# Optimization experiments

Measured on AMD Instinct MI355X. Metric: run time of the kernel, lower is better.

## Reference

```python
import jax, jax.numpy as jnp
import numpy as np

B, SQ, SKV, D, DC, R, H = 4, 2048, 2048, 1024, 1024, 4, 16


def setup_inputs() -> dict:
    key = jax.random.key(0)
    ks = jax.random.split(key, 15)
    s = 0.02
    return {
        "hidden_states": jax.random.normal(ks[0], (B, SQ, D), jnp.float32),
        "encoder_hidden_states": jax.random.normal(ks[1], (B, SKV, DC), jnp.float32),
        "Wq": jax.random.normal(ks[2], (D, D), jnp.float32) * s,
        "Wk": jax.random.normal(ks[3], (DC, D), jnp.float32) * s,
        "Wv": jax.random.normal(ks[4], (DC, D), jnp.float32) * s,
        "Wo": jax.random.normal(ks[5], (D, D), jnp.float32) * s,
        "bo": jax.random.normal(ks[6], (D,), jnp.float32) * s,
        "q_lora_down": jax.random.normal(ks[7], (D, R), jnp.float32) * s,
        "q_lora_up": jax.random.normal(ks[8], (R, D), jnp.float32) * s,
        "k_lora_down": jax.random.normal(ks[9], (DC, R), jnp.float32) * s,
        "k_lora_up": jax.random.normal(ks[10], (R, D), jnp.float32) * s,
        "v_lora_down": jax.random.normal(ks[11], (DC, R), jnp.float32) * s,
        "v_lora_up": jax.random.normal(ks[12], (R, D), jnp.float32) * s,
        "out_lora_down": jax.random.normal(ks[13], (D, R), jnp.float32) * s,
        "out_lora_up": jax.random.normal(ks[14], (R, D), jnp.float32) * s,
        "n_heads": H,
    }


def reference(hidden_states, encoder_hidden_states, Wq, Wk, Wv, Wo, bo,
              q_lora_down, q_lora_up, k_lora_down, k_lora_up,
              v_lora_down, v_lora_up, out_lora_down, out_lora_up, n_heads):
    b, sq, d = hidden_states.shape
    skv = encoder_hidden_states.shape[1]
    hd = d // n_heads
    scale = 1.0 / jnp.sqrt(jnp.asarray(hd, hidden_states.dtype))

    # Q/K/V projections with LoRA adapters (bias-free, diffusers style)
    q = hidden_states @ Wq + (hidden_states @ q_lora_down) @ q_lora_up
    k = encoder_hidden_states @ Wk + (encoder_hidden_states @ k_lora_down) @ k_lora_up
    v = encoder_hidden_states @ Wv + (encoder_hidden_states @ v_lora_down) @ v_lora_up

    q = q.reshape(b, sq, n_heads, hd)
    k = k.reshape(b, skv, n_heads, hd)
    v = v.reshape(b, skv, n_heads, hd)

    # get_attention_scores: scaled QK^T + softmax (no mask)
    scores = jnp.einsum("bqhd,bkhd->bhqk", q, k) * scale
    probs = jax.nn.softmax(scores, axis=-1)

    out = jnp.einsum("bhqk,bkhd->bqhd", probs, v).reshape(b, sq, d)

    # to_out[0] linear + LoRA on the pre-projection residual; to_out[1] dropout is identity
    residual = out
    out = out @ Wo + bo + (residual @ out_lora_down) @ out_lora_up
    return out
```

## Files before the change

### kernel.cpp

```cpp
#include <hip/hip_runtime.h>
#include <hip/hip_bf16.h>

typedef __attribute__((ext_vector_type(8))) short bf16x8;
typedef __attribute__((ext_vector_type(4))) float f32x4;

#define DEVFN static __device__ __forceinline__

constexpr int kSQ = 2048, kSKV = 2048, kD = 1024, kH = 16;
constexpr int kM = 4 * kSQ;

DEVFN unsigned short f2bf(float f) {
  union { float f; unsigned u; } v; v.f = f;
  unsigned r = v.u + 0x7FFFu + ((v.u >> 16) & 1u);
  return (unsigned short)(r >> 16);
}
DEVFN float bf2f(unsigned short h) {
  union { unsigned u; float f; } v; v.u = ((unsigned)h) << 16; return v.f;
}
DEVFN unsigned cvtpk(float lo, float hi) {
  unsigned r;
  asm("v_cvt_pk_bf16_f32 %0, %1, %2" : "=v"(r) : "v"(lo), "v"(hi));
  return r;
}
DEVFN float vexp2(float x) {
  float r;
  asm("v_exp_f32 %0, %1" : "=v"(r) : "v"(x));
  return r;
}

DEVFN void gload16(const void* g, void* l) {
  __builtin_amdgcn_global_load_lds(
      (const __attribute__((address_space(1))) unsigned int*)g,
      (__attribute__((address_space(3))) unsigned int*)l, 16, 0, 0);
}

#define WT12 asm volatile("s_waitcnt vmcnt(12)" ::: "memory")
#define WT6  asm volatile("s_waitcnt vmcnt(6)" ::: "memory")
#define WT0  asm volatile("s_waitcnt vmcnt(0)" ::: "memory")

__global__ __launch_bounds__(256) void k_prep_wt(
    const float* __restrict__ hs, const float* __restrict__ enc,
    const float* __restrict__ Wq, const float* __restrict__ Wk,
    const float* __restrict__ Wv, const float* __restrict__ Wo,
    unsigned short* __restrict__ hsb, unsigned short* __restrict__ encb,
    unsigned short* __restrict__ Wqt, unsigned short* __restrict__ Wkvt,
    unsigned short* __restrict__ Wot) {
  __shared__ unsigned short tile[64][65];
  const int bid = blockIdx.x;
  const int tid = threadIdx.x;

  if (bid < 2 * kM) {
    const bool isH = bid < kM;
    const int rr = isH ? bid : bid - kM;
    const float* srcRow = (isH ? hs : enc) + (size_t)rr * kD;
    unsigned short* dstRow = (isH ? hsb : encb) + (size_t)rr * kD;
    float4 x = reinterpret_cast<const float4*>(srcRow)[tid];
    short4 o;
    o.x = (short)f2bf(x.x); o.y = (short)f2bf(x.y);
    o.z = (short)f2bf(x.z); o.w = (short)f2bf(x.w);
    *reinterpret_cast<short4*>(dstRow + tid * 4) = o;
  } else {
    const int t = bid - 2 * kM;
    const int wid = t >> 8, tt = t & 255;
    const float* W = (wid == 0) ? Wq : (wid == 1) ? Wk : (wid == 2) ? Wv : Wo;
    unsigned short* Wt = (wid == 0) ? Wqt : (wid == 1) ? Wkvt
                        : (wid == 2) ? (Wkvt + (size_t)1024 * 1024) : Wot;
    const int tk0 = (tt & 15) * 64;
    const int tn0 = (tt >> 4) * 64;
    for (int i = tid; i < 4096; i += 256) {
      int r = i >> 6, c = i & 63;
      tile[r][c] = f2bf(W[(size_t)(tk0 + r) * 1024 + tn0 + c]);
    }
    __syncthreads();
    for (int i = tid; i < 4096; i += 256) {
      int r = i >> 6, c = i & 63;
      Wt[(size_t)(tn0 + r) * 1024 + tk0 + c] = tile[c][r];
    }
  }
}

__global__ __launch_bounds__(256) void k_lora(
    const unsigned short* __restrict__ X,
    const float* __restrict__ dn0, const float* __restrict__ dn1,
    float* __restrict__ tout, int tstr) {
  __shared__ unsigned short DNT[16][1032];
  const int tid = threadIdx.x;
  const int rbase = (int)blockIdx.x * 64;
  for (int i = tid; i < 16 * 1032; i += 256) DNT[i / 1032][i % 1032] = 0;
  __syncthreads();
  for (int i = tid; i < 4096; i += 256) {
    const int k = i >> 2, c = i & 3;
    DNT[c][k] = f2bf(dn0[i]);
  }
  if (dn1 != nullptr) {
    for (int i = tid; i < 4096; i += 256) {
      const int k = i >> 2, c = i & 3;
      DNT[4 + c][k] = f2bf(dn1[i]);
    }
  }
  __syncthreads();
  const int l = tid & 63, w = tid >> 6;
  const int lr = l & 15, lk = l >> 4;
  const unsigned short* Xr = X + (size_t)(rbase + w * 16 + lr) * 1024 + lk * 8;
  const f32x4 zero = {0.f, 0.f, 0.f, 0.f};
  f32x4 acc0 = zero, acc1 = zero;
#pragma unroll 4
  for (int k0 = 0; k0 < 1024; k0 += 64) {
    bf16x8 a0 = *(const bf16x8*)(Xr + k0);
    bf16x8 b0 = *(const bf16x8*)&DNT[lr][k0 + lk * 8];
    bf16x8 a1 = *(const bf16x8*)(Xr + k0 + 32);
    bf16x8 b1 = *(const bf16x8*)&DNT[lr][k0 + 32 + lk * 8];
    acc0 = __builtin_amdgcn_mfma_f32_16x16x32_bf16(a0, b0, acc0, 0, 0, 0);
    acc1 = __builtin_amdgcn_mfma_f32_16x16x32_bf16(a1, b1, acc1, 0, 0, 0);
  }
  if (lr < tstr) {
#pragma unroll
    for (int r = 0; r < 4; ++r) {
      const int grow = rbase + w * 16 + lk * 4 + r;
      tout[(size_t)grow * tstr + lr] = acc0[r] + acc1[r];
    }
  }
}


#define GSTAGE(dbuf, kt) do {                                                 \
    _Pragma("unroll")                                                         \
    for (int j = 0; j < 4; ++j) {                                             \
      const int s = (j * 8 + w) * 64 + l;                                     \
      const int row = s >> 3, u = s & 7;                                      \
      gload16(Ap + (size_t)row * 1024 + (kt) * 64 + ((u ^ (row & 7)) * 8),    \
              &lA[dbuf][(j * 8 + w) * 512]);                                  \
    }                                                                         \
    _Pragma("unroll")                                                         \
    for (int j = 0; j < 2; ++j) {                                             \
      const int s = (j * 8 + w) * 64 + l;                                     \
      const int row = s >> 3, u = s & 7;                                      \
      gload16(Bp + (size_t)row * 1024 + (kt) * 64 + ((u ^ (row & 7)) * 8),    \
              &lB[dbuf][(j * 8 + w) * 512]);                                  \
    } } while (0)

#define BIG_GEMM_LOOP(TRANS)                                                  \
  GSTAGE(0, 0);                                                               \
  GSTAGE(1, 1);                                                               \
  GSTAGE(2, 2);                                                               \
  _Pragma("unroll")                                                           \
  for (int kt = 0; kt < 16; ++kt) {                                           \
    const int cur = kt % 3;                                                   \
    if (kt <= 13) { WT12; } else if (kt == 14) { WT6; } else { WT0; }         \
    __builtin_amdgcn_s_barrier();                                             \
    asm volatile("" ::: "memory");                                            \
    _Pragma("unroll")                                                         \
    for (int kk = 0; kk < 2; ++kk) {                                          \
      bf16x8 af[8], bfr[2];                                                   \
      _Pragma("unroll")                                                       \
      for (int m = 0; m < 8; ++m) {                                           \
        const int ar = wr + m * 16 + lr;                                      \
        af[m] = *(const bf16x8*)&lA[cur][ar * 64 +                            \
                 (((kk * 4 + lk) ^ (ar & 7)) * 8)];                           \
      }                                                                       \
      _Pragma("unroll")                                                       \
      for (int n = 0; n < 2; ++n) {                                           \
        const int br = wc + n * 16 + lr;                                      \
        bfr[n] = *(const bf16x8*)&lB[cur][br * 64 +                           \
                 (((kk * 4 + lk) ^ (br & 7)) * 8)];                           \
      }                                                                       \
      __builtin_amdgcn_s_setprio(1);                                          \
      _Pragma("unroll")                                                       \
      for (int m = 0; m < 8; ++m)                                             \
        _Pragma("unroll")                                                     \
        for (int n = 0; n < 2; ++n)                                           \
          acc[m][n] = (TRANS)                                                 \
            ? __builtin_amdgcn_mfma_f32_16x16x32_bf16(bfr[n], af[m],          \
                                                      acc[m][n], 0, 0, 0)     \
            : __builtin_amdgcn_mfma_f32_16x16x32_bf16(af[m], bfr[n],          \
                                                      acc[m][n], 0, 0, 0);    \
      __builtin_amdgcn_s_setprio(0);                                          \
    }                                                                         \
    asm volatile("s_waitcnt lgkmcnt(0)" ::: "memory");                        \
    __builtin_amdgcn_s_barrier();                                             \
    asm volatile("" ::: "memory");                                            \
    if (kt < 13) GSTAGE(cur, kt + 3);                                         \
  }

__global__ __launch_bounds__(512, 2) void k_gemm_qkv(
    const unsigned short* __restrict__ hsb, const unsigned short* __restrict__ encb,
    const unsigned short* __restrict__ Wqt, const unsigned short* __restrict__ Wkvt,
    const float* __restrict__ tq, const float* __restrict__ tkv,
    const float* __restrict__ q_up, const float* __restrict__ k_up,
    const float* __restrict__ v_up,
    unsigned short* __restrict__ Qhp, unsigned short* __restrict__ Khp,
    unsigned short* __restrict__ Vhp) {
  __shared__ unsigned short lA[3][256 * 64];
  __shared__ unsigned short lB[3][128 * 64];
  const int tid = threadIdx.x;
  const int l = tid & 63, w = tid >> 6;
  const int bid = blockIdx.x;

  const unsigned short *A, *Bt;
  const float *tmat, *up;
  unsigned short* dst;
  int m0, nB0, nOut0, tstr;
  if (bid < 256) {
    const int rid = (bid & 7) * 32 + (bid >> 3);
    m0 = (rid >> 3) * 256; nB0 = (rid & 7) * 128;
    A = hsb; Bt = Wqt; tmat = tq; tstr = 4; up = q_up; dst = Qhp; nOut0 = nB0;
  } else {
    const int b2 = bid - 256;
    const int rid = (b2 & 7) * 64 + (b2 >> 3);
    m0 = (rid >> 4) * 256; nB0 = (rid & 15) * 128;
    A = encb; Bt = Wkvt; tstr = 8;
    if (nB0 < 1024) { tmat = tkv;     up = k_up; dst = Khp; nOut0 = nB0; }
    else            { tmat = tkv + 4; up = v_up; dst = Vhp; nOut0 = nB0 - 1024; }
  }
  const int wr = (w >> 2) * 128, wc = (w & 3) * 32;
  const int lr = l & 15, lk = l >> 4;
  const unsigned short* Ap = A  + (size_t)m0  * 1024;
  const unsigned short* Bp = Bt + (size_t)nB0 * 1024;

  f32x4 acc[8][2];
  const f32x4 zero = {0.f, 0.f, 0.f, 0.f};
#pragma unroll
  for (int m = 0; m < 8; ++m)
#pragma unroll
    for (int n = 0; n < 2; ++n) acc[m][n] = zero;

  BIG_GEMM_LOOP(1)

  unsigned short* rep = &lA[0][0];
#pragma unroll
  for (int n = 0; n < 2; ++n) {
    const int cb = wc + n * 16 + lk * 4;
    const float4 u0v = *reinterpret_cast<const float4*>(&up[nOut0 + cb]);
    const float4 u1v = *reinterpret_cast<const float4*>(&up[1024 + nOut0 + cb]);
    const float4 u2v = *reinterpret_cast<const float4*>(&up[2048 + nOut0 + cb]);
    const float4 u3v = *reinterpret_cast<const float4*>(&up[3072 + nOut0 + cb]);
    const int u16 = cb >> 3;
    const int bo8 = (lk & 1) * 8;
#pragma unroll
    for (int m = 0; m < 8; ++m) {
      const int row = wr + m * 16 + lr;
      const int grow = m0 + row;
      const float4 tt = *reinterpret_cast<const float4*>(tmat + (size_t)grow * tstr);
      const float v0 = acc[m][n][0] + tt.x * u0v.x + tt.y * u1v.x + tt.z * u2v.x + tt.w * u3v.x;
      const float v1 = acc[m][n][1] + tt.x * u0v.y + tt.y * u1v.y + tt.z * u2v.y + tt.w * u3v.y;
      const float v2 = acc[m][n][2] + tt.x * u0v.z + tt.y * u1v.z + tt.z * u2v.z + tt.w * u3v.z;
      const float v3 = acc[m][n][3] + tt.x * u0v.w + tt.y * u1v.w + tt.z * u2v.w + tt.w * u3v.w;
      uint2 pk; pk.x = cvtpk(v0, v1); pk.y = cvtpk(v2, v3);
      *(uint2*)((char*)rep + row * 256 + ((u16 ^ (row & 7)) << 4) + bo8) = pk;
    }
  }
  __syncthreads();
  const int sub = l & 7;
#pragma unroll
  for (int it = 0; it < 8; ++it) {
    const int g = w * 64 + it * 8 + (l >> 3);
    const int head = g >> 8, row = g & 255;
    const int ju = ((head * 8 + sub) ^ (row & 7)) << 4;
    uint4 val = *(const uint4*)((const char*)rep + row * 256 + ju);
    const int grow = m0 + row;
    const int b = grow >> 11, s = grow & 2047;
    const int hg = (nOut0 >> 6) + head;
    *(uint4*)&dst[(((size_t)(b * kH + hg)) * 2048 + s) * 64 + sub * 8] = val;
  }
}

__global__ __launch_bounds__(512, 2) void k_gemm_out(
    const unsigned short* __restrict__ A, const unsigned short* __restrict__ Bt,
    const float* __restrict__ tmat, const float* __restrict__ up,
    const float* __restrict__ bias, float* __restrict__ outp) {
  __shared__ unsigned short lA[3][256 * 64];
  __shared__ unsigned short lB[3][128 * 64];
  const int tid = threadIdx.x;
  const int l = tid & 63, w = tid >> 6;
  const int bid = blockIdx.x;
  const int rid = (bid & 7) * 32 + (bid >> 3);
  const int m0 = (rid >> 3) * 256, nB0 = (rid & 7) * 128;
  const int wr = (w >> 2) * 128, wc = (w & 3) * 32;
  const int lr = l & 15, lk = l >> 4;
  const unsigned short* Ap = A  + (size_t)m0  * 1024;
  const unsigned short* Bp = Bt + (size_t)nB0 * 1024;

  f32x4 acc[8][2];
  const f32x4 zero = {0.f, 0.f, 0.f, 0.f};
#pragma unroll
  for (int m = 0; m < 8; ++m)
#pragma unroll
    for (int n = 0; n < 2; ++n) acc[m][n] = zero;

  BIG_GEMM_LOOP(0)

#pragma unroll
  for (int n = 0; n < 2; ++n) {
    const int gcol = nB0 + wc + n * 16 + lr;
    const float u0 = up[gcol], u1 = up[1024 + gcol];
    const float u2 = up[2048 + gcol], u3 = up[3072 + gcol];
    const float bz = bias[gcol];
#pragma unroll
    for (int m = 0; m < 8; ++m) {
#pragma unroll
      for (int r = 0; r < 4; ++r) {
        const int grow = m0 + wr + m * 16 + lk * 4 + r;
        const float4 tt = *reinterpret_cast<const float4*>(tmat + (size_t)grow * 4);
        outp[(size_t)grow * 1024 + gcol] =
            acc[m][n][r] + tt.x * u0 + tt.y * u1 + tt.z * u2 + tt.w * u3 + bz;
      }
    }
  }
}

__global__ __launch_bounds__(256) void k_vt(const unsigned short* __restrict__ Vh,
                                            unsigned short* __restrict__ Vt) {
  __shared__ unsigned short tile[64][65];
  const int bh = blockIdx.y;
  const int s0 = blockIdx.x * 64;
  const unsigned short* src = Vh + ((size_t)bh * kSKV + s0) * 64;
  for (int i = threadIdx.x; i < 4096; i += 256) {
    int r = i >> 6, c = i & 63;
    tile[r][c] = src[(size_t)r * 64 + c];
  }
  __syncthreads();
  unsigned short* dst = Vt + (size_t)bh * 64 * kSKV + s0;
  for (int i = threadIdx.x; i < 4096; i += 256) {
    int r = i >> 6, c = i & 63;
    dst[(size_t)r * kSKV + c] = tile[c][r];
  }
}

__global__ __launch_bounds__(256) void k_attn(
    const unsigned short* __restrict__ Qh, const unsigned short* __restrict__ Kh,
    const unsigned short* __restrict__ Vt, unsigned short* __restrict__ Obf) {
  __shared__ unsigned short lK[2][4096];
  __shared__ unsigned short lV[2][4096];
  __shared__ __align__(16) unsigned short lP[4][1024];

  const int bid = blockIdx.x + 16 * blockIdx.y;
  const int rid = (bid & 7) * 128 + (bid >> 3);
  const int q0 = (rid & 15) * 128;
  const int bh = rid >> 4;

  const int tid = threadIdx.x;
  const int l = tid & 63, w = tid >> 6;
  const int lr = l & 15, lk = l >> 4;
  const int m7 = lr & 7;
  const int lkh = lk >> 1, lkb = lk & 1;

  const unsigned short* Qb = Qh + (size_t)bh * kSQ * 64;
  const unsigned short* Kb = Kh + (size_t)bh * kSKV * 64;
  const unsigned short* Vb = Vt + (size_t)bh * 64 * kSKV;

  const float QS = 0.125f * 1.4426950408889634f;
  bf16x8 qf[2][2];
#pragma unroll
  for (int m = 0; m < 2; ++m)
#pragma unroll
    for (int kk = 0; kk < 2; ++kk) {
      bf16x8 v = *(const bf16x8*)
          &Qb[(size_t)(q0 + w * 32 + m * 16 + lr) * 64 + kk * 32 + lk * 8];
#pragma unroll
      for (int j = 0; j < 8; ++j) {
        unsigned short u = (unsigned short)v[j];
        v[j] = (short)f2bf(bf2f(u) * QS);
      }
      qf[m][kk] = v;
    }

  f32x4 oacc[2][4];
  const f32x4 zero = {0.f, 0.f, 0.f, 0.f};
#pragma unroll
  for (int m = 0; m < 2; ++m)
#pragma unroll
    for (int n = 0; n < 4; ++n) oacc[m][n] = zero;
  float lrow[2] = {0.f, 0.f};

  const int sr8 = l >> 3;
  const int su = (l & 7) ^ sr8;
  unsigned short* lPw = lP[w];

#define ASTAGE(dbuf, tile) do { \
    _Pragma("unroll") for (int cc = 0; cc < 2; ++cc) { \
      const int c = 2 * w + cc; const int row = c * 8 + sr8; \
      gload16(Kb + (size_t)((tile) * 64 + row) * 64 + su * 8, &lK[dbuf][c * 512]); \
      gload16(Vb + (size_t)row * kSKV + (tile) * 64 + su * 8, &lV[dbuf][c * 512]); \
    } } while (0)

  ASTAGE(0, 0);
  __syncthreads();

#pragma unroll 2
  for (int kt = 0; kt < 32; ++kt) {
    const int cur = kt & 1;
    if (kt < 31) ASTAGE(cur ^ 1, kt + 1);
    const unsigned short* bufK = lK[cur];
    const unsigned short* bufV = lV[cur];

    bf16x8 kf[4][2];
#pragma unroll
    for (int n = 0; n < 4; ++n)
#pragma unroll
      for (int kk = 0; kk < 2; ++kk) {
        const int ub = (kk * 4 + lk) ^ m7;
        kf[n][kk] = *(const bf16x8*)&bufK[(n * 16 + lr) * 64 + ub * 8];
      }

    f32x4 s0[4];
#pragma unroll
    for (int n = 0; n < 4; ++n) s0[n] = zero;
    __builtin_amdgcn_s_setprio(1);
#pragma unroll
    for (int kk = 0; kk < 2; ++kk)
#pragma unroll
      for (int n = 0; n < 4; ++n)
        s0[n] = __builtin_amdgcn_mfma_f32_16x16x32_bf16(kf[n][kk], qf[0][kk],
                                                        s0[n], 0, 0, 0);
    __builtin_amdgcn_s_setprio(0);
    float ls0 = 0.f;
#pragma unroll
    for (int n = 0; n < 4; ++n) {
      const float p0 = vexp2(s0[n][0]);
      const float p1 = vexp2(s0[n][1]);
      const float p2 = vexp2(s0[n][2]);
      const float p3 = vexp2(s0[n][3]);
      ls0 += (p0 + p1) + (p2 + p3);
      uint2 pv; pv.x = cvtpk(p0, p1); pv.y = cvtpk(p2, p3);
      *(uint2*)&lPw[lr * 64 + (((2 * n + lkh) ^ m7) << 3) + lkb * 4] = pv;
    }
    lrow[0] += ls0;

    f32x4 s1[4];
#pragma unroll
    for (int n = 0; n < 4; ++n) s1[n] = zero;
    __builtin_amdgcn_s_setprio(1);
#pragma unroll
    for (int kk = 0; kk < 2; ++kk)
#pragma unroll
      for (int n = 0; n < 4; ++n)
        s1[n] = __builtin_amdgcn_mfma_f32_16x16x32_bf16(kf[n][kk], qf[1][kk],
                                                        s1[n], 0, 0, 0);
    __builtin_amdgcn_s_setprio(0);
    float ls1 = 0.f;
    uint2 pw1[4];
#pragma unroll
    for (int n = 0; n < 4; ++n) {
      const float p0 = vexp2(s1[n][0]);
      const float p1 = vexp2(s1[n][1]);
      const float p2 = vexp2(s1[n][2]);
      const float p3 = vexp2(s1[n][3]);
      ls1 += (p0 + p1) + (p2 + p3);
      pw1[n].x = cvtpk(p0, p1); pw1[n].y = cvtpk(p2, p3);
    }
    lrow[1] += ls1;

    bf16x8 pf0[2], pf1[2];
#pragma unroll
    for (int kk = 0; kk < 2; ++kk)
      pf0[kk] = *(const bf16x8*)&lPw[lr * 64 + (((kk * 4 + lk) ^ m7) << 3)];
#pragma unroll
    for (int n = 0; n < 4; ++n)
      *(uint2*)&lPw[lr * 64 + (((2 * n + lkh) ^ m7) << 3) + lkb * 4] = pw1[n];
#pragma unroll
    for (int kk = 0; kk < 2; ++kk)
      pf1[kk] = *(const bf16x8*)&lPw[lr * 64 + (((kk * 4 + lk) ^ m7) << 3)];

    __builtin_amdgcn_s_setprio(1);
#pragma unroll
    for (int n = 0; n < 4; ++n)
#pragma unroll
      for (int kk = 0; kk < 2; ++kk) {
        const int ub = (kk * 4 + lk) ^ m7;
        bf16x8 vf = *(const bf16x8*)&bufV[(n * 16 + lr) * 64 + ub * 8];
        oacc[0][n] = __builtin_amdgcn_mfma_f32_16x16x32_bf16(pf0[kk], vf,
                                                             oacc[0][n], 0, 0, 0);
        oacc[1][n] = __builtin_amdgcn_mfma_f32_16x16x32_bf16(pf1[kk], vf,
                                                             oacc[1][n], 0, 0, 0);
      }
    __builtin_amdgcn_s_setprio(0);

    __syncthreads();
  }
#undef ASTAGE

  float rinv[2][4];
#pragma unroll
  for (int m = 0; m < 2; ++m) {
    float s = lrow[m];
    s += __shfl_xor(s, 16);
    s += __shfl_xor(s, 32);
#pragma unroll
    for (int r = 0; r < 4; ++r) rinv[m][r] = 1.0f / __shfl(s, lk * 4 + r);
  }

  const int b = bh >> 4, h = bh & 15;
#pragma unroll
  for (int m = 0; m < 2; ++m)
#pragma unroll
    for (int n = 0; n < 4; ++n)
#pragma unroll
      for (int r = 0; r < 4; ++r) {
        const int qrow = q0 + w * 32 + m * 16 + lk * 4 + r;
        const int d = n * 16 + lr;
        Obf[((size_t)b * kSQ + qrow) * kD + h * 64 + d] =
            f2bf(oacc[m][n][r] * rinv[m][r]);
      }
}

extern "C" void kernel_launch(void* const* d_in, const int* in_sizes, int n_in,
                              void* d_out, int out_size, void* d_ws, size_t ws_size,
                              hipStream_t stream) {
  (void)in_sizes; (void)n_in; (void)out_size; (void)ws_size;
  const float* hs   = (const float*)d_in[0];
  const float* enc  = (const float*)d_in[1];
  const float* Wq   = (const float*)d_in[2];
  const float* Wk   = (const float*)d_in[3];
  const float* Wv   = (const float*)d_in[4];
  const float* Wo   = (const float*)d_in[5];
  const float* bo   = (const float*)d_in[6];
  const float* q_dn = (const float*)d_in[7];
  const float* q_up = (const float*)d_in[8];
  const float* k_dn = (const float*)d_in[9];
  const float* k_up = (const float*)d_in[10];
  const float* v_dn = (const float*)d_in[11];
  const float* v_up = (const float*)d_in[12];
  const float* o_dn = (const float*)d_in[13];
  const float* o_up = (const float*)d_in[14];

  char* ws = (char*)d_ws;
  size_t off = 0;
  auto alloc = [&](size_t bytes) -> void* {
    void* p = ws + off;
    off += (bytes + 255) & ~(size_t)255;
    return p;
  };
  const size_t ACT = (size_t)kM * kD * 2;
  unsigned short* hsb  = (unsigned short*)alloc(ACT);
  unsigned short* encb = (unsigned short*)alloc(ACT);
  unsigned short* Wqt  = (unsigned short*)alloc((size_t)1024 * 1024 * 2);
  unsigned short* Wkvt = (unsigned short*)alloc((size_t)2048 * 1024 * 2);
  unsigned short* Wot  = (unsigned short*)alloc((size_t)1024 * 1024 * 2);
  unsigned short* Qhp  = (unsigned short*)alloc(ACT);
  unsigned short* Khp  = (unsigned short*)alloc(ACT);
  unsigned short* Vhp  = (unsigned short*)alloc(ACT);
  float* tq  = (float*)alloc((size_t)kM * 4 * 4);
  float* tkv = (float*)alloc((size_t)kM * 8 * 4);
  float* to  = (float*)alloc((size_t)kM * 4 * 4);
  unsigned short* Vtt = hsb;
  unsigned short* Ob  = encb;

  k_prep_wt<<<dim3(2 * kM + 1024), dim3(256), 0, stream>>>(
      hs, enc, Wq, Wk, Wv, Wo, hsb, encb, Wqt, Wkvt, Wot);

  k_lora<<<dim3(128), dim3(256), 0, stream>>>(hsb, q_dn, (const float*)nullptr,
                                              tq, 4);
  k_lora<<<dim3(128), dim3(256), 0, stream>>>(encb, k_dn, v_dn, tkv, 8);

  k_gemm_qkv<<<dim3(768), dim3(512), 0, stream>>>(
      hsb, encb, Wqt, Wkvt, tq, tkv, q_up, k_up, v_up, Qhp, Khp, Vhp);

  k_vt<<<dim3(32, 64), dim3(256), 0, stream>>>(Vhp, Vtt);
  k_attn<<<dim3(16, 64), dim3(256), 0, stream>>>(Qhp, Khp, Vtt, Ob);

  k_lora<<<dim3(128), dim3(256), 0, stream>>>(Ob, o_dn, (const float*)nullptr,
                                              to, 4);

  k_gemm_out<<<dim3(256), dim3(512), 0, stream>>>(Ob, Wot, to, o_up, bo,
                                                  (float*)d_out);
}
```

Before: 245.4 us.

## Double attention query tile per block to 256 rows, halving K/V reloads

Each attention workgroup now handles 256 query rows (64 per wave) instead of 128, so each staged K/V tile is reused by four 16-row query fragments per wave and total K/V global traffic is halved. The grid shrinks from 1024 to 512 blocks with a new block-to-(head, q-tile) remap, and launch bounds request two blocks per CU. The cost is roughly double the accumulator and Q-fragment registers, fewer blocks to fill the GPU, and loss of the explicit loop unroll.

Result: faster. 232.8 us (median of 2 runs) (-5.1%).

```diff
diff --git a/kernel.cpp b/kernel.cpp
--- a/kernel.cpp
+++ b/kernel.cpp
@@ -326,17 +326,17 @@
   }
 }
 
-__global__ __launch_bounds__(256) void k_attn(
+__global__ __launch_bounds__(256, 2) void k_attn(
     const unsigned short* __restrict__ Qh, const unsigned short* __restrict__ Kh,
     const unsigned short* __restrict__ Vt, unsigned short* __restrict__ Obf) {
   __shared__ unsigned short lK[2][4096];
   __shared__ unsigned short lV[2][4096];
   __shared__ __align__(16) unsigned short lP[4][1024];
 
-  const int bid = blockIdx.x + 16 * blockIdx.y;
-  const int rid = (bid & 7) * 128 + (bid >> 3);
-  const int q0 = (rid & 15) * 128;
-  const int bh = rid >> 4;
+  const int bid = blockIdx.x;
+  const int rid = (bid & 7) * 64 + (bid >> 3);
+  const int q0 = (rid & 7) * 256;
+  const int bh = rid >> 3;
 
   const int tid = threadIdx.x;
   const int l = tid & 63, w = tid >> 6;
@@ -349,13 +349,13 @@
   const unsigned short* Vb = Vt + (size_t)bh * 64 * kSKV;
 
   const float QS = 0.125f * 1.4426950408889634f;
-  bf16x8 qf[2][2];
-#pragma unroll
-  for (int m = 0; m < 2; ++m)
+  bf16x8 qf[4][2];
+#pragma unroll
+  for (int m = 0; m < 4; ++m)
 #pragma unroll
     for (int kk = 0; kk < 2; ++kk) {
       bf16x8 v = *(const bf16x8*)
-          &Qb[(size_t)(q0 + w * 32 + m * 16 + lr) * 64 + kk * 32 + lk * 8];
+          &Qb[(size_t)(q0 + w * 64 + m * 16 + lr) * 64 + kk * 32 + lk * 8];
 #pragma unroll
       for (int j = 0; j < 8; ++j) {
         unsigned short u = (unsigned short)v[j];
@@ -364,13 +364,13 @@
       qf[m][kk] = v;
     }
 
-  f32x4 oacc[2][4];
+  f32x4 oacc[4][4];
   const f32x4 zero = {0.f, 0.f, 0.f, 0.f};
 #pragma unroll
-  for (int m = 0; m < 2; ++m)
+  for (int m = 0; m < 4; ++m)
 #pragma unroll
     for (int n = 0; n < 4; ++n) oacc[m][n] = zero;
-  float lrow[2] = {0.f, 0.f};
+  float lrow[4] = {0.f, 0.f, 0.f, 0.f};
 
   const int sr8 = l >> 3;
   const int su = (l & 7) ^ sr8;
@@ -386,7 +386,6 @@
   ASTAGE(0, 0);
   __syncthreads();
 
-#pragma unroll 2
   for (int kt = 0; kt < 32; ++kt) {
     const int cur = kt & 1;
     if (kt < 31) ASTAGE(cur ^ 1, kt + 1);
@@ -402,64 +401,68 @@
         kf[n][kk] = *(const bf16x8*)&bufK[(n * 16 + lr) * 64 + ub * 8];
       }
 
-    f32x4 s0[4];
-#pragma unroll
-    for (int n = 0; n < 4; ++n) s0[n] = zero;
-    __builtin_amdgcn_s_setprio(1);
-#pragma unroll
-    for (int kk = 0; kk < 2; ++kk)
+    bf16x8 pf[4][2];
+#pragma unroll
+    for (int mp = 0; mp < 2; ++mp) {
+      const int ma = mp * 2, mb = mp * 2 + 1;
+      f32x4 s0[4];
+#pragma unroll
+      for (int n = 0; n < 4; ++n) s0[n] = zero;
+      __builtin_amdgcn_s_setprio(1);
+#pragma unroll
+      for (int kk = 0; kk < 2; ++kk)
+#pragma unroll
+        for (int n = 0; n < 4; ++n)
+          s0[n] = __builtin_amdgcn_mfma_f32_16x16x32_bf16(kf[n][kk], qf[ma][kk],
+                                                          s0[n], 0, 0, 0);
+      __builtin_amdgcn_s_setprio(0);
+      float ls0 = 0.f;
+#pragma unroll
+      for (int n = 0; n < 4; ++n) {
+        const float p0 = vexp2(s0[n][0]);
+        const float p1 = vexp2(s0[n][1]);
+        const float p2 = vexp2(s0[n][2]);
+        const float p3 = vexp2(s0[n][3]);
+        ls0 += (p0 + p1) + (p2 + p3);
+        uint2 pv; pv.x = cvtpk(p0, p1); pv.y = cvtpk(p2, p3);
+        *(uint2*)&lPw[lr * 64 + (((2 * n + lkh) ^ m7) << 3) + lkb * 4] = pv;
+      }
+      lrow[ma] += ls0;
+
+      f32x4 s1[4];
+#pragma unroll
+      for (int n = 0; n < 4; ++n) s1[n] = zero;
+      __builtin_amdgcn_s_setprio(1);
+#pragma unroll
+      for (int kk = 0; kk < 2; ++kk)
+#pragma unroll
+        for (int n = 0; n < 4; ++n)
+          s1[n] = __builtin_amdgcn_mfma_f32_16x16x32_bf16(kf[n][kk], qf[mb][kk],
+                                                          s1[n], 0, 0, 0);
+      __builtin_amdgcn_s_setprio(0);
+      float ls1 = 0.f;
+      uint2 pw1[4];
+#pragma unroll
+      for (int n = 0; n < 4; ++n) {
+        const float p0 = vexp2(s1[n][0]);
+        const float p1 = vexp2(s1[n][1]);
+        const float p2 = vexp2(s1[n][2]);
+        const float p3 = vexp2(s1[n][3]);
+        ls1 += (p0 + p1) + (p2 + p3);
+        pw1[n].x = cvtpk(p0, p1); pw1[n].y = cvtpk(p2, p3);
+      }
+      lrow[mb] += ls1;
+
+#pragma unroll
+      for (int kk = 0; kk < 2; ++kk)
+        pf[ma][kk] = *(const bf16x8*)&lPw[lr * 64 + (((kk * 4 + lk) ^ m7) << 3)];
 #pragma unroll
       for (int n = 0; n < 4; ++n)
-        s0[n] = __builtin_amdgcn_mfma_f32_16x16x32_bf16(kf[n][kk], qf[0][kk],
-                                                        s0[n], 0, 0, 0);
-    __builtin_amdgcn_s_setprio(0);
-    float ls0 = 0.f;
-#pragma unroll
-    for (int n = 0; n < 4; ++n) {
-      const float p0 = vexp2(s0[n][0]);
-      const float p1 = vexp2(s0[n][1]);
-      const float p2 = vexp2(s0[n][2]);
-      const float p3 = vexp2(s0[n][3]);
-      ls0 += (p0 + p1) + (p2 + p3);
-      uint2 pv; pv.x = cvtpk(p0, p1); pv.y = cvtpk(p2, p3);
-      *(uint2*)&lPw[lr * 64 + (((2 * n + lkh) ^ m7) << 3) + lkb * 4] = pv;
-    }
-    lrow[0] += ls0;
-
-    f32x4 s1[4];
-#pragma unroll
-    for (int n = 0; n < 4; ++n) s1[n] = zero;
-    __builtin_amdgcn_s_setprio(1);
-#pragma unroll
-    for (int kk = 0; kk < 2; ++kk)
-#pragma unroll
-      for (int n = 0; n < 4; ++n)
-        s1[n] = __builtin_amdgcn_mfma_f32_16x16x32_bf16(kf[n][kk], qf[1][kk],
-                                                        s1[n], 0, 0, 0);
-    __builtin_amdgcn_s_setprio(0);
-    float ls1 = 0.f;
-    uint2 pw1[4];
-#pragma unroll
-    for (int n = 0; n < 4; ++n) {
-      const float p0 = vexp2(s1[n][0]);
-      const float p1 = vexp2(s1[n][1]);
-      const float p2 = vexp2(s1[n][2]);
-      const float p3 = vexp2(s1[n][3]);
-      ls1 += (p0 + p1) + (p2 + p3);
-      pw1[n].x = cvtpk(p0, p1); pw1[n].y = cvtpk(p2, p3);
-    }
-    lrow[1] += ls1;
-
-    bf16x8 pf0[2], pf1[2];
-#pragma unroll
-    for (int kk = 0; kk < 2; ++kk)
-      pf0[kk] = *(const bf16x8*)&lPw[lr * 64 + (((kk * 4 + lk) ^ m7) << 3)];
-#pragma unroll
-    for (int n = 0; n < 4; ++n)
-      *(uint2*)&lPw[lr * 64 + (((2 * n + lkh) ^ m7) << 3) + lkb * 4] = pw1[n];
-#pragma unroll
-    for (int kk = 0; kk < 2; ++kk)
-      pf1[kk] = *(const bf16x8*)&lPw[lr * 64 + (((kk * 4 + lk) ^ m7) << 3)];
+        *(uint2*)&lPw[lr * 64 + (((2 * n + lkh) ^ m7) << 3) + lkb * 4] = pw1[n];
+#pragma unroll
+      for (int kk = 0; kk < 2; ++kk)
+        pf[mb][kk] = *(const bf16x8*)&lPw[lr * 64 + (((kk * 4 + lk) ^ m7) << 3)];
+    }
 
     __builtin_amdgcn_s_setprio(1);
 #pragma unroll
@@ -468,10 +471,10 @@
       for (int kk = 0; kk < 2; ++kk) {
         const int ub = (kk * 4 + lk) ^ m7;
         bf16x8 vf = *(const bf16x8*)&bufV[(n * 16 + lr) * 64 + ub * 8];
-        oacc[0][n] = __builtin_amdgcn_mfma_f32_16x16x32_bf16(pf0[kk], vf,
-                                                             oacc[0][n], 0, 0, 0);
-        oacc[1][n] = __builtin_amdgcn_mfma_f32_16x16x32_bf16(pf1[kk], vf,
-                                                             oacc[1][n], 0, 0, 0);
+#pragma unroll
+        for (int m = 0; m < 4; ++m)
+          oacc[m][n] = __builtin_amdgcn_mfma_f32_16x16x32_bf16(pf[m][kk], vf,
+                                                               oacc[m][n], 0, 0, 0);
       }
     __builtin_amdgcn_s_setprio(0);
 
@@ -479,9 +482,9 @@
   }
 #undef ASTAGE
 
-  float rinv[2][4];
-#pragma unroll
-  for (int m = 0; m < 2; ++m) {
+  float rinv[4][4];
+#pragma unroll
+  for (int m = 0; m < 4; ++m) {
     float s = lrow[m];
     s += __shfl_xor(s, 16);
     s += __shfl_xor(s, 32);
@@ -491,12 +494,12 @@
 
   const int b = bh >> 4, h = bh & 15;
 #pragma unroll
-  for (int m = 0; m < 2; ++m)
+  for (int m = 0; m < 4; ++m)
 #pragma unroll
     for (int n = 0; n < 4; ++n)
 #pragma unroll
       for (int r = 0; r < 4; ++r) {
-        const int qrow = q0 + w * 32 + m * 16 + lk * 4 + r;
+        const int qrow = q0 + w * 64 + m * 16 + lk * 4 + r;
         const int d = n * 16 + lr;
         Obf[((size_t)b * kSQ + qrow) * kD + h * 64 + d] =
             f2bf(oacc[m][n][r] * rinv[m][r]);
@@ -556,7 +559,7 @@
       hsb, encb, Wqt, Wkvt, tq, tkv, q_up, k_up, v_up, Qhp, Khp, Vhp);
 
   k_vt<<<dim3(32, 64), dim3(256), 0, stream>>>(Vhp, Vtt);
-  k_attn<<<dim3(16, 64), dim3(256), 0, stream>>>(Qhp, Khp, Vtt, Ob);
+  k_attn<<<dim3(512), dim3(256), 0, stream>>>(Qhp, Khp, Vtt, Ob);
 
   k_lora<<<dim3(128), dim3(256), 0, stream>>>(Ob, o_dn, (const float*)nullptr,
                                               to, 4);
```
